# Kernel optimization log

Measured on AMD Instinct MI355X. Metric: run time of the kernel, lower is better.

## Reference

```python
import jax, jax.numpy as jnp
import numpy as np

N, E, D_IN, H, L, C = 50000, 800000, 500, 256, 4, 7
ALPHA, GAMMA, EPS = 0.5, 0.5, 0.1  # self-loop weight, parallel-edge weight, FAConv eps
LN_EPS = 1e-5


def setup_inputs() -> dict:
    key = jax.random.key(0)
    ks = jax.random.split(key, 8)
    x = jax.random.normal(ks[0], (N, D_IN), jnp.float32)
    src = jax.random.randint(ks[1], (E,), 0, N, jnp.int32)
    dst = jax.random.randint(ks[2], (E,), 0, N, jnp.int32)
    dst = jnp.where(dst == src, (dst + 1) % N, dst)  # ensure no self-loops (remove_self_loops is then a no-op)
    edge_index = jnp.stack([src, dst])
    s_in = 1.0 / np.sqrt(D_IN)
    s_h = 1.0 / np.sqrt(H)
    W_init = jax.random.uniform(ks[3], (H, D_IN), jnp.float32, -s_in, s_in)
    b_init = jnp.zeros((H,), jnp.float32)
    att_l = jax.random.uniform(ks[4], (L, H), jnp.float32, -s_h, s_h)
    att_r = jax.random.uniform(ks[5], (L, H), jnp.float32, -s_h, s_h)
    ln_g = jnp.ones((L, H), jnp.float32)
    ln_b = jnp.zeros((L, H), jnp.float32)
    W_last = jax.random.uniform(ks[6], (C, H), jnp.float32, -s_h, s_h)
    b_last = jnp.zeros((C,), jnp.float32)
    return dict(x=x, edge_index=edge_index, W_init=W_init, b_init=b_init,
                att_l=att_l, att_r=att_r, ln_g=ln_g, ln_b=ln_b,
                W_last=W_last, b_last=b_last)


def _layernorm(x, g, b):
    mu = jnp.mean(x, axis=-1, keepdims=True)
    var = jnp.var(x, axis=-1, keepdims=True)
    return (x - mu) * jax.lax.rsqrt(var + LN_EPS) * g + b


def reference(x, edge_index, W_init, b_init, att_l, att_r, ln_g, ln_b, W_last, b_last):
    num_nodes = x.shape[0]
    num_edges = edge_index.shape[1]
    x = x @ W_init.T + b_init  # [N, H]
    x0 = x
    # add self-loops after parallel edges
    loop = jnp.arange(num_nodes, dtype=edge_index.dtype)
    src = jnp.concatenate([edge_index[0], loop])
    dst = jnp.concatenate([edge_index[1], loop])
    ew = jnp.concatenate([jnp.full((num_edges,), GAMMA, x.dtype),
                          jnp.full((num_nodes,), ALPHA, x.dtype)])
    for i in range(L):
        # FAConv: alpha_e = tanh(att_l.x_src + att_r.x_dst); msg = x_src * alpha_e * ew
        al = x @ att_l[i]  # [N]
        ar = x @ att_r[i]  # [N]
        a_e = jnp.tanh(al[src] + ar[dst]) * ew  # [E+N]
        msg = x[src] * a_e[:, None]            # [E+N, H]
        agg = jax.ops.segment_sum(msg, dst, num_segments=num_nodes)
        x = agg + EPS * x0
        if i != L - 1:
            x = _layernorm(jax.nn.relu(x), ln_g[i], ln_b[i])
            # F.dropout with p=0.0 is identity
    emb = x @ W_last.T + b_last  # [N, C]
    return emb, jax.nn.log_softmax(emb, axis=1)
```

## Files before the change

kernel.cpp:

```cpp
#include <hip/hip_runtime.h>
#include <hip/hip_fp16.h>

#define N_NODES 50000
#define N_EDGES 800000
#define D_IN_K  500
#define K_PAD   512
#define H_DIM   256
#define N_CLS   7
#define ALPHA_W 0.5f
#define GAMMA_W 0.5f
#define EPS_W   0.1f
#define LN_EPS_W 1e-5f

#define SCAN_B 256
#define SCAN_NB ((N_NODES + SCAN_B - 1) / SCAN_B)

typedef unsigned short u16;
typedef unsigned int   u32;
typedef _Float16 f16;
typedef __attribute__((ext_vector_type(8))) _Float16 f16x8;
typedef __attribute__((ext_vector_type(4))) float    f32x4;
typedef __attribute__((ext_vector_type(8))) unsigned short u16x8;

__device__ __forceinline__ float h2f(u16 v) {
    __half h;
    *reinterpret_cast<u16*>(&h) = v;
    return __half2float(h);
}
__device__ __forceinline__ u16 f2h(float f) {
    __half h = __float2half_rn(f);
    return *reinterpret_cast<u16*>(&h);
}
__device__ __forceinline__ int clampN(int v) {
    return (v < 0) ? 0 : ((v >= N_NODES) ? N_NODES - 1 : v);
}

__device__ __forceinline__ void fma_mix_row(float* acc, u16x8 v, float c) {
    uint4 p = *reinterpret_cast<const uint4*>(&v);
    asm("v_fma_mix_f32 %0, %1, %2, %0 op_sel:[0,0,0] op_sel_hi:[1,0,0]" : "+v"(acc[0]) : "v"(p.x), "v"(c));
    asm("v_fma_mix_f32 %0, %1, %2, %0 op_sel:[1,0,0] op_sel_hi:[1,0,0]" : "+v"(acc[1]) : "v"(p.x), "v"(c));
    asm("v_fma_mix_f32 %0, %1, %2, %0 op_sel:[0,0,0] op_sel_hi:[1,0,0]" : "+v"(acc[2]) : "v"(p.y), "v"(c));
    asm("v_fma_mix_f32 %0, %1, %2, %0 op_sel:[1,0,0] op_sel_hi:[1,0,0]" : "+v"(acc[3]) : "v"(p.y), "v"(c));
    asm("v_fma_mix_f32 %0, %1, %2, %0 op_sel:[0,0,0] op_sel_hi:[1,0,0]" : "+v"(acc[4]) : "v"(p.z), "v"(c));
    asm("v_fma_mix_f32 %0, %1, %2, %0 op_sel:[1,0,0] op_sel_hi:[1,0,0]" : "+v"(acc[5]) : "v"(p.z), "v"(c));
    asm("v_fma_mix_f32 %0, %1, %2, %0 op_sel:[0,0,0] op_sel_hi:[1,0,0]" : "+v"(acc[6]) : "v"(p.w), "v"(c));
    asm("v_fma_mix_f32 %0, %1, %2, %0 op_sel:[1,0,0] op_sel_hi:[1,0,0]" : "+v"(acc[7]) : "v"(p.w), "v"(c));
}

__global__ __launch_bounds__(256) void sentinel_kernel(float* out, int n) {
    int i = blockIdx.x * blockDim.x + threadIdx.x;
    if (i < n) out[i] = 2.0f;
}

__global__ __launch_bounds__(256) void zero_kernel(int* p, int n) {
    int i = blockIdx.x * blockDim.x + threadIdx.x;
    if (i < n) p[i] = 0;
}

__global__ __launch_bounds__(256) void hist_kernel(const int* __restrict__ dst, int* __restrict__ deg, int e) {
    int i = blockIdx.x * blockDim.x + threadIdx.x;
    if (i < e) atomicAdd(&deg[clampN(dst[i])], 1);
}

__global__ __launch_bounds__(SCAN_B) void scan_a(const int* __restrict__ deg, int* __restrict__ row_ptr,
                                                 int* __restrict__ bsum) {
    __shared__ int sdata[SCAN_B];
    int t = threadIdx.x;
    int i = blockIdx.x * SCAN_B + t;
    int v = (i < N_NODES) ? deg[i] : 0;
    sdata[t] = v;
    __syncthreads();
#pragma unroll
    for (int off = 1; off < SCAN_B; off <<= 1) {
        int a = (t >= off) ? sdata[t - off] : 0;
        __syncthreads();
        sdata[t] += a;
        __syncthreads();
    }
    if (i < N_NODES) row_ptr[i] = sdata[t] - v;
    if (t == SCAN_B - 1) bsum[blockIdx.x] = sdata[t];
}

__global__ __launch_bounds__(SCAN_B) void scan_b(int* __restrict__ bsum, int* __restrict__ boff,
                                                 int* __restrict__ row_ptr) {
    __shared__ int sdata[SCAN_B];
    int t = threadIdx.x;
    int v = (t < SCAN_NB) ? bsum[t] : 0;
    sdata[t] = v;
    __syncthreads();
#pragma unroll
    for (int off = 1; off < SCAN_B; off <<= 1) {
        int a = (t >= off) ? sdata[t - off] : 0;
        __syncthreads();
        sdata[t] += a;
        __syncthreads();
    }
    if (t < SCAN_NB) boff[t] = sdata[t] - v;
    if (t == SCAN_B - 1) row_ptr[N_NODES] = sdata[t];
}

__global__ __launch_bounds__(SCAN_B) void scan_c(int* __restrict__ row_ptr, const int* __restrict__ boff) {
    int i = blockIdx.x * SCAN_B + threadIdx.x;
    if (i < N_NODES) row_ptr[i] += boff[blockIdx.x];
}

__global__ __launch_bounds__(256) void scatter_kernel(const int* __restrict__ src, const int* __restrict__ dst,
                                                      const int* __restrict__ row_ptr, int* __restrict__ deg,
                                                      int* __restrict__ srcS, int e) {
    int i = blockIdx.x * blockDim.x + threadIdx.x;
    if (i < e) {
        int d = clampN(dst[i]);
        int old = atomicSub(&deg[d], 1);
        int pos = row_ptr[d] + old - 1;
        if (pos >= 0 && pos < e) srcS[pos] = clampN(src[i]);
    }
}

__global__ __launch_bounds__(256) void convert_w(const float* __restrict__ W, f16* __restrict__ W16) {
    int i = blockIdx.x * 256 + threadIdx.x;
    int n = i >> 9, k = i & (K_PAD - 1);
    W16[i] = (k < D_IN_K) ? (f16)W[n * D_IN_K + k] : (f16)0.f;
}

#define GW_STRIDE 520
#define GA_BUF    (16 * GW_STRIDE)

__device__ __forceinline__ f16x8 stage_load(const float* __restrict__ X, int tile, int r, int sc) {
    const float* p = X + (long)(tile * 16 + r) * D_IN_K + sc;
    f16x8 v;
    if (sc + 8 <= D_IN_K) {
        float4 lo = *(const float4*)(p);
        float4 hi = *(const float4*)(p + 4);
        v[0] = (f16)lo.x; v[1] = (f16)lo.y; v[2] = (f16)lo.z; v[3] = (f16)lo.w;
        v[4] = (f16)hi.x; v[5] = (f16)hi.y; v[6] = (f16)hi.z; v[7] = (f16)hi.w;
    } else {
#pragma unroll
        for (int t = 0; t < 8; t++)
            v[t] = (sc + t < D_IN_K) ? (f16)p[t] : (f16)0.f;
    }
    return v;
}

__global__ __launch_bounds__(1024) void mfma_gemm5(const float* __restrict__ X,
                                                   const f16* __restrict__ W16,
                                                   const float* __restrict__ bias,
                                                   u16* __restrict__ out) {
    __shared__ __align__(16) f16 alds[2 * GA_BUF];

    int tid  = threadIdx.x;
    int w    = tid >> 6;
    int lane = tid & 63;
    int m    = lane & 15;
    int quad = lane >> 4;
    int h    = w * 16 + m;

    f16x8 bfrag[16];
    {
        const f16* wb = W16 + (long)h * K_PAD + quad * 8;
#pragma unroll
        for (int kc = 0; kc < 16; kc++)
            bfrag[kc] = *(const f16x8*)(wb + kc * 32);
    }
    float bv = bias[h];

    int sr = w;
    int sc = lane * 8;

    int nt = N_NODES / 16;
    int t  = blockIdx.x;
    int buf = 0;

    if (t < nt) {
        f16x8 sv = stage_load(X, t, sr, sc);
        *(f16x8*)&alds[sr * GW_STRIDE + sc] = sv;
    }
    __syncthreads();

    while (t < nt) {
        int tn = t + (int)gridDim.x;
        bool hn = (tn < nt);
        f16x8 nsv;
        if (hn) nsv = stage_load(X, tn, sr, sc);

        f32x4 acc = (f32x4){0.f, 0.f, 0.f, 0.f};
        const f16* ab = &alds[buf * GA_BUF + m * GW_STRIDE + quad * 8];
#pragma unroll
        for (int kc = 0; kc < 16; kc++) {
            f16x8 a = *(const f16x8*)(ab + kc * 32);
            acc = __builtin_amdgcn_mfma_f32_16x16x32_f16(a, bfrag[kc], acc, 0, 0, 0);
        }

        long nb = (long)t * 16 + quad * 4;
#pragma unroll
        for (int r = 0; r < 4; r++)
            out[(nb + r) * H_DIM + h] = f2h(acc[r] + bv);

        if (hn) *(f16x8*)&alds[(buf ^ 1) * GA_BUF + sr * GW_STRIDE + sc] = nsv;
        __syncthreads();
        buf ^= 1;
        t = tn;
    }
}

__global__ __launch_bounds__(256) void alar_kernel(const u16* __restrict__ x,
                                                   const float* __restrict__ attl,
                                                   const float* __restrict__ attr,
                                                   float* __restrict__ al, float* __restrict__ ar, int n) {
    int w = (blockIdx.x * blockDim.x + threadIdx.x) >> 6;
    int lane = threadIdx.x & 63;
    if (w >= n) return;
    int col = lane * 4;
    ushort4 xv = *(const ushort4*)(x + (long)w * H_DIM + col);
    float4 lv = *(const float4*)(attl + col);
    float4 rv = *(const float4*)(attr + col);
    float x0 = h2f(xv.x), x1 = h2f(xv.y), x2 = h2f(xv.z), x3 = h2f(xv.w);
    float pl = x0 * lv.x + x1 * lv.y + x2 * lv.z + x3 * lv.w;
    float pr = x0 * rv.x + x1 * rv.y + x2 * rv.z + x3 * rv.w;
#pragma unroll
    for (int off = 32; off >= 1; off >>= 1) {
        pl += __shfl_xor(pl, off);
        pr += __shfl_xor(pr, off);
    }
    if (lane == 0) { al[w] = pl; ar[w] = pr; }
}

__global__ __launch_bounds__(256) void layer_kernel5(const u16* __restrict__ xin,
                                                     const u16* __restrict__ x0,
                                                     const float* __restrict__ alIn,
                                                     float* __restrict__ alOut,
                                                     float* __restrict__ ar,
                                                     const int* __restrict__ row_ptr,
                                                     const int* __restrict__ srcS,
                                                     const float* __restrict__ g,
                                                     const float* __restrict__ b,
                                                     const float* __restrict__ attlN,
                                                     const float* __restrict__ attrN,
                                                     u16* __restrict__ xout,
                                                     const float* __restrict__ Wl,
                                                     const float* __restrict__ bl,
                                                     float* __restrict__ outF,
                                                     int n, int mode) {
    int pair = (blockIdx.x * 256 + threadIdx.x) >> 6;
    int lane = threadIdx.x & 63;
    int half = lane >> 5;
    int sub  = lane & 31;
    int w = pair * 2 + half;
    if (w >= n) w = n - 1;
    int col = sub * 8;

    float arn = ar[w];
    float aself = ALPHA_W * tanhf(alIn[w] + arn);

    float acc[8];
    {
        u16x8 xs  = *(const u16x8*)(xin + (long)w * H_DIM + col);
        u16x8 x0v = *(const u16x8*)(x0  + (long)w * H_DIM + col);
#pragma unroll
        for (int k = 0; k < 8; k++) acc[k] = aself * h2f(xs[k]) + EPS_W * h2f(x0v[k]);
    }

    int e0 = row_ptr[w], e1 = row_ptr[w + 1];
    int d  = e1 - e0;
    int dmax = max(d, __shfl(d, lane ^ 32));

    for (int cb = 0; cb < dmax; cb += 32) {
        int cnt  = d - cb;
        int cmax = dmax - cb; if (cmax > 32) cmax = 32;
        int s = 0; float a = 0.f;
        if (sub < cnt) {
            s = clampN(srcS[e0 + cb + sub]);
            a = GAMMA_W * tanhf(alIn[s] + arn);
        }
        int hb = half << 5;
        for (int j = 0; j < cmax; j += 4) {
            int   s0 = __shfl(s, hb + j),     s1 = __shfl(s, hb + j + 1);
            int   s2 = __shfl(s, hb + j + 2), s3 = __shfl(s, hb + j + 3);
            float c0 = __shfl(a, hb + j),     c1 = __shfl(a, hb + j + 1);
            float c2 = __shfl(a, hb + j + 2), c3 = __shfl(a, hb + j + 3);
            u16x8 v0 = *(const u16x8*)(xin + (long)s0 * H_DIM + col);
            u16x8 v1 = *(const u16x8*)(xin + (long)s1 * H_DIM + col);
            u16x8 v2 = *(const u16x8*)(xin + (long)s2 * H_DIM + col);
            u16x8 v3 = *(const u16x8*)(xin + (long)s3 * H_DIM + col);
            fma_mix_row(acc, v0, c0);
            fma_mix_row(acc, v1, c1);
            fma_mix_row(acc, v2, c2);
            fma_mix_row(acc, v3, c3);
        }
    }

    if (mode == 0) {
        float v[8];
        float sum = 0.f, sq = 0.f;
#pragma unroll
        for (int k = 0; k < 8; k++) {
            v[k] = fmaxf(acc[k], 0.f);
            sum += v[k];
            sq  += v[k] * v[k];
        }
#pragma unroll
        for (int off = 16; off >= 1; off >>= 1) {
            sum += __shfl_xor(sum, off);
            sq  += __shfl_xor(sq, off);
        }
        float mu = sum * (1.f / 256.f);
        float var = fmaxf(sq * (1.f / 256.f) - mu * mu, 0.f);
        float rstd = rsqrtf(var + LN_EPS_W);
        float4 ga = *(const float4*)(g + col);
        float4 gb = *(const float4*)(g + col + 4);
        float4 ba = *(const float4*)(b + col);
        float4 bb = *(const float4*)(b + col + 4);
        float gg[8]  = {ga.x, ga.y, ga.z, ga.w, gb.x, gb.y, gb.z, gb.w};
        float bbv[8] = {ba.x, ba.y, ba.z, ba.w, bb.x, bb.y, bb.z, bb.w};
        float4 la = *(const float4*)(attlN + col);
        float4 lb = *(const float4*)(attlN + col + 4);
        float4 ra = *(const float4*)(attrN + col);
        float4 rb = *(const float4*)(attrN + col + 4);
        float ll[8] = {la.x, la.y, la.z, la.w, lb.x, lb.y, lb.z, lb.w};
        float rr[8] = {ra.x, ra.y, ra.z, ra.w, rb.x, rb.y, rb.z, rb.w};
        float pl = 0.f, pr = 0.f;
        u16x8 o;
#pragma unroll
        for (int k = 0; k < 8; k++) {
            float val = (v[k] - mu) * rstd * gg[k] + bbv[k];
            o[k] = f2h(val);
            pl += val * ll[k];
            pr += val * rr[k];
        }
#pragma unroll
        for (int off = 16; off >= 1; off >>= 1) {
            pl += __shfl_xor(pl, off);
            pr += __shfl_xor(pr, off);
        }
        if (sub == 0) { alOut[w] = pl; ar[w] = pr; }
        *(u16x8*)(xout + (long)w * H_DIM + col) = o;
    } else {
        float p[N_CLS];
#pragma unroll
        for (int c = 0; c < N_CLS; c++) {
            const float* wr = Wl + c * H_DIM + col;
            float4 wa = *(const float4*)(wr);
            float4 wb = *(const float4*)(wr + 4);
            p[c] = acc[0] * wa.x + acc[1] * wa.y + acc[2] * wa.z + acc[3] * wa.w
                 + acc[4] * wb.x + acc[5] * wb.y + acc[6] * wb.z + acc[7] * wb.w;
        }
#pragma unroll
        for (int off = 16; off >= 1; off >>= 1) {
#pragma unroll
            for (int c = 0; c < N_CLS; c++) p[c] += __shfl_xor(p[c], off);
        }
        if (sub == 0) {
            float e[N_CLS];
            float m = -1e30f;
#pragma unroll
            for (int c = 0; c < N_CLS; c++) {
                e[c] = p[c] + bl[c];
                m = fmaxf(m, e[c]);
            }
            float sx = 0.f;
#pragma unroll
            for (int c = 0; c < N_CLS; c++) sx += expf(e[c] - m);
            float lse = logf(sx);
#pragma unroll
            for (int c = 0; c < N_CLS; c++) {
                outF[(long)w * N_CLS + c] = e[c];
                outF[(long)N_NODES * N_CLS + (long)w * N_CLS + c] = e[c] - m - lse;
            }
        }
    }
}

extern "C" void kernel_launch(void* const* d_in, const int* in_sizes, int n_in,
                              void* d_out, int out_size, void* d_ws, size_t ws_size,
                              hipStream_t stream) {
    const float* x_in   = (const float*)d_in[0];
    const int*   ei     = (const int*)d_in[1];
    const float* W_init = (const float*)d_in[2];
    const float* b_init = (const float*)d_in[3];
    const float* att_l  = (const float*)d_in[4];
    const float* att_r  = (const float*)d_in[5];
    const float* ln_g   = (const float*)d_in[6];
    const float* ln_b   = (const float*)d_in[7];
    const float* W_last = (const float*)d_in[8];
    const float* b_last = (const float*)d_in[9];
    float* out = (float*)d_out;

    const size_t OFF_X0  = 0;
    const size_t OFF_XA  = 25600000;
    const size_t OFF_XB  = 51200000;
    const size_t OFF_AL  = 76800000;
    const size_t OFF_AR  = 77000000;
    const size_t OFF_DEG = 77200000;
    const size_t OFF_RP  = 77400000;
    const size_t OFF_SRC = 77600064;
    const size_t OFF_BS  = 80800064;
    const size_t OFF_BO  = 80801088;
    const size_t WS_NEED = 80802112;

    if (ws_size < WS_NEED) {
        sentinel_kernel<<<(out_size + 255) / 256, 256, 0, stream>>>(out, out_size);
        return;
    }

    char* ws = (char*)d_ws;
    u16* x0  = (u16*)(ws + OFF_X0);
    u16* xA  = (u16*)(ws + OFF_XA);
    u16* xB  = (u16*)(ws + OFF_XB);
    f16* W16 = (f16*)(ws + OFF_AL);
    float* al  = (float*)(ws + OFF_AL);
    float* ar  = (float*)(ws + OFF_AR);
    float* al2 = (float*)(ws + OFF_DEG);
    int* deg     = (int*)(ws + OFF_DEG);
    int* row_ptr = (int*)(ws + OFF_RP);
    int* srcS    = (int*)(ws + OFF_SRC);
    int* bsum    = (int*)(ws + OFF_BS);
    int* boff    = (int*)(ws + OFF_BO);

    const int* e_src = ei;
    const int* e_dst = ei + N_EDGES;

    int zb = (N_NODES + 255) / 256;
    zero_kernel<<<zb, 256, 0, stream>>>(deg, N_NODES);
    int eb = (N_EDGES + 255) / 256;
    hist_kernel<<<eb, 256, 0, stream>>>(e_dst, deg, N_EDGES);
    scan_a<<<SCAN_NB, SCAN_B, 0, stream>>>(deg, row_ptr, bsum);
    scan_b<<<1, SCAN_B, 0, stream>>>(bsum, boff, row_ptr);
    scan_c<<<SCAN_NB, SCAN_B, 0, stream>>>(row_ptr, boff);
    scatter_kernel<<<eb, 256, 0, stream>>>(e_src, e_dst, row_ptr, deg, srcS, N_EDGES);

    convert_w<<<(H_DIM * K_PAD) / 256, 256, 0, stream>>>(W_init, W16);
    mfma_gemm5<<<256, 1024, 0, stream>>>(x_in, W16, b_init, x0);

    int nb = (N_NODES * 64 + 255) / 256;
    alar_kernel<<<nb, 256, 0, stream>>>(x0, att_l, att_r, al, ar, N_NODES);

    int lb = (N_NODES + 7) / 8;
    const u16* bufs_in[4]   = {x0, xA, xB, xA};
    u16* bufs_out[4]        = {xA, xB, xA, xB};
    const float* al_in[4]   = {al, al2, al, al2};
    float* al_out[4]        = {al2, al, al2, al};
    for (int i = 0; i < 4; i++) {
        int nxt = (i < 3) ? (i + 1) : i;
        layer_kernel5<<<lb, 256, 0, stream>>>(bufs_in[i], x0, al_in[i], al_out[i], ar,
                                              row_ptr, srcS,
                                              ln_g + i * H_DIM, ln_b + i * H_DIM,
                                              att_l + nxt * H_DIM, att_r + nxt * H_DIM,
                                              bufs_out[i], W_last, b_last, out,
                                              N_NODES, (i < 3) ? 0 : 1);
    }
}
```

Baseline: 522.8 us.

## Fuse three-kernel scan into one block; triple-buffer GEMM input staging

The three-pass prefix scan over node degrees is replaced by one 1024-thread block. Each thread serially scans a chunk of about 49 entries, which removes two kernel launches. The input GEMM now prefetches raw fp32 rows two tiles ahead into registers, using a three-slot LDS ring with a single barrier per iteration, to hide global load latency behind MFMA work. The risks are a serial single-block scan with uncoalesced strided reads, plus extra register and LDS pressure in the GEMM.

```diff
diff --git a/kernel.cpp b/kernel.cpp
--- a/kernel.cpp
+++ b/kernel.cpp
@@ -12,9 +12,6 @@
 #define EPS_W   0.1f
 #define LN_EPS_W 1e-5f
 
-#define SCAN_B 256
-#define SCAN_NB ((N_NODES + SCAN_B - 1) / SCAN_B)
-
 typedef unsigned short u16;
 typedef unsigned int   u32;
 typedef _Float16 f16;
@@ -62,46 +59,30 @@
     if (i < e) atomicAdd(&deg[clampN(dst[i])], 1);
 }
 
-__global__ __launch_bounds__(SCAN_B) void scan_a(const int* __restrict__ deg, int* __restrict__ row_ptr,
-                                                 int* __restrict__ bsum) {
-    __shared__ int sdata[SCAN_B];
+__global__ __launch_bounds__(1024) void scan_fused(const int* __restrict__ deg, int* __restrict__ row_ptr) {
+    __shared__ int sdata[1024];
     int t = threadIdx.x;
-    int i = blockIdx.x * SCAN_B + t;
-    int v = (i < N_NODES) ? deg[i] : 0;
-    sdata[t] = v;
+    const int CH = (N_NODES + 1023) / 1024;
+    int beg = t * CH;
+    int end = beg + CH; if (end > N_NODES) end = N_NODES;
+    int s = 0;
+    for (int j = beg; j < end; j++) s += deg[j];
+    sdata[t] = s;
     __syncthreads();
 #pragma unroll
-    for (int off = 1; off < SCAN_B; off <<= 1) {
+    for (int off = 1; off < 1024; off <<= 1) {
         int a = (t >= off) ? sdata[t - off] : 0;
         __syncthreads();
         sdata[t] += a;
         __syncthreads();
     }
-    if (i < N_NODES) row_ptr[i] = sdata[t] - v;
-    if (t == SCAN_B - 1) bsum[blockIdx.x] = sdata[t];
-}
-
-__global__ __launch_bounds__(SCAN_B) void scan_b(int* __restrict__ bsum, int* __restrict__ boff,
-                                                 int* __restrict__ row_ptr) {
-    __shared__ int sdata[SCAN_B];
-    int t = threadIdx.x;
-    int v = (t < SCAN_NB) ? bsum[t] : 0;
-    sdata[t] = v;
-    __syncthreads();
-#pragma unroll
-    for (int off = 1; off < SCAN_B; off <<= 1) {
-        int a = (t >= off) ? sdata[t - off] : 0;
-        __syncthreads();
-        sdata[t] += a;
-        __syncthreads();
-    }
-    if (t < SCAN_NB) boff[t] = sdata[t] - v;
-    if (t == SCAN_B - 1) row_ptr[N_NODES] = sdata[t];
-}
-
-__global__ __launch_bounds__(SCAN_B) void scan_c(int* __restrict__ row_ptr, const int* __restrict__ boff) {
-    int i = blockIdx.x * SCAN_B + threadIdx.x;
-    if (i < N_NODES) row_ptr[i] += boff[blockIdx.x];
+    int run = sdata[t] - s;
+    for (int j = beg; j < end; j++) {
+        int d = deg[j];
+        row_ptr[j] = run;
+        run += d;
+    }
+    if (t == 1023) row_ptr[N_NODES] = sdata[1023];
 }
 
 __global__ __launch_bounds__(256) void scatter_kernel(const int* __restrict__ src, const int* __restrict__ dst,
@@ -125,27 +106,32 @@
 #define GW_STRIDE 520
 #define GA_BUF    (16 * GW_STRIDE)
 
-__device__ __forceinline__ f16x8 stage_load(const float* __restrict__ X, int tile, int r, int sc) {
+__device__ __forceinline__ void raw_load(const float* __restrict__ X, int tile, int r, int sc,
+                                         float4& lo, float4& hi) {
     const float* p = X + (long)(tile * 16 + r) * D_IN_K + sc;
+    if (sc + 8 <= D_IN_K) {
+        lo = *(const float4*)(p);
+        hi = *(const float4*)(p + 4);
+    } else if (sc < D_IN_K) {
+        lo = *(const float4*)(p);
+        hi = make_float4(0.f, 0.f, 0.f, 0.f);
+    } else {
+        lo = make_float4(0.f, 0.f, 0.f, 0.f);
+        hi = make_float4(0.f, 0.f, 0.f, 0.f);
+    }
+}
+__device__ __forceinline__ f16x8 cvt8(float4 lo, float4 hi) {
     f16x8 v;
-    if (sc + 8 <= D_IN_K) {
-        float4 lo = *(const float4*)(p);
-        float4 hi = *(const float4*)(p + 4);
-        v[0] = (f16)lo.x; v[1] = (f16)lo.y; v[2] = (f16)lo.z; v[3] = (f16)lo.w;
-        v[4] = (f16)hi.x; v[5] = (f16)hi.y; v[6] = (f16)hi.z; v[7] = (f16)hi.w;
-    } else {
-#pragma unroll
-        for (int t = 0; t < 8; t++)
-            v[t] = (sc + t < D_IN_K) ? (f16)p[t] : (f16)0.f;
-    }
+    v[0] = (f16)lo.x; v[1] = (f16)lo.y; v[2] = (f16)lo.z; v[3] = (f16)lo.w;
+    v[4] = (f16)hi.x; v[5] = (f16)hi.y; v[6] = (f16)hi.z; v[7] = (f16)hi.w;
     return v;
 }
 
-__global__ __launch_bounds__(1024) void mfma_gemm5(const float* __restrict__ X,
+__global__ __launch_bounds__(1024) void mfma_gemm6(const float* __restrict__ X,
                                                    const f16* __restrict__ W16,
                                                    const float* __restrict__ bias,
                                                    u16* __restrict__ out) {
-    __shared__ __align__(16) f16 alds[2 * GA_BUF];
+    __shared__ __align__(16) f16 alds[3 * GA_BUF];
 
     int tid  = threadIdx.x;
     int w    = tid >> 6;
@@ -166,21 +152,26 @@
     int sr = w;
     int sc = lane * 8;
 
-    int nt = N_NODES / 16;
-    int t  = blockIdx.x;
-    int buf = 0;
-
-    if (t < nt) {
-        f16x8 sv = stage_load(X, t, sr, sc);
-        *(f16x8*)&alds[sr * GW_STRIDE + sc] = sv;
-    }
-    __syncthreads();
-
+    const int nt = N_NODES / 16;
+    const int G  = (int)gridDim.x;
+    int t = blockIdx.x;
+
+    {
+        float4 lo, hi;
+        raw_load(X, t, sr, sc, lo, hi);
+        *(f16x8*)&alds[sr * GW_STRIDE + sc] = cvt8(lo, hi);
+    }
+    float4 lo1, hi1;
+    bool h1 = (t + G < nt);
+    if (h1) raw_load(X, t + G, sr, sc, lo1, hi1);
+
+    int buf = 0, nbuf = 1;
     while (t < nt) {
-        int tn = t + (int)gridDim.x;
-        bool hn = (tn < nt);
-        f16x8 nsv;
-        if (hn) nsv = stage_load(X, tn, sr, sc);
+        bool h2 = (t + 2 * G < nt);
+        float4 lo2, hi2;
+        if (h2) raw_load(X, t + 2 * G, sr, sc, lo2, hi2);
+        if (h1) *(f16x8*)&alds[nbuf * GA_BUF + sr * GW_STRIDE + sc] = cvt8(lo1, hi1);
+        __syncthreads();
 
         f32x4 acc = (f32x4){0.f, 0.f, 0.f, 0.f};
         const f16* ab = &alds[buf * GA_BUF + m * GW_STRIDE + quad * 8];
@@ -189,16 +180,14 @@
             f16x8 a = *(const f16x8*)(ab + kc * 32);
             acc = __builtin_amdgcn_mfma_f32_16x16x32_f16(a, bfrag[kc], acc, 0, 0, 0);
         }
-
         long nb = (long)t * 16 + quad * 4;
 #pragma unroll
         for (int r = 0; r < 4; r++)
             out[(nb + r) * H_DIM + h] = f2h(acc[r] + bv);
 
-        if (hn) *(f16x8*)&alds[(buf ^ 1) * GA_BUF + sr * GW_STRIDE + sc] = nsv;
-        __syncthreads();
-        buf ^= 1;
-        t = tn;
+        lo1 = lo2; hi1 = hi2; h1 = h2;
+        t += G;
+        buf = nbuf; nbuf = (nbuf + 1) % 3;
     }
 }
 
@@ -412,8 +401,6 @@
     int* deg     = (int*)(ws + OFF_DEG);
     int* row_ptr = (int*)(ws + OFF_RP);
     int* srcS    = (int*)(ws + OFF_SRC);
-    int* bsum    = (int*)(ws + OFF_BS);
-    int* boff    = (int*)(ws + OFF_BO);
 
     const int* e_src = ei;
     const int* e_dst = ei + N_EDGES;
@@ -422,13 +409,11 @@
     zero_kernel<<<zb, 256, 0, stream>>>(deg, N_NODES);
     int eb = (N_EDGES + 255) / 256;
     hist_kernel<<<eb, 256, 0, stream>>>(e_dst, deg, N_EDGES);
-    scan_a<<<SCAN_NB, SCAN_B, 0, stream>>>(deg, row_ptr, bsum);
-    scan_b<<<1, SCAN_B, 0, stream>>>(bsum, boff, row_ptr);
-    scan_c<<<SCAN_NB, SCAN_B, 0, stream>>>(row_ptr, boff);
+    scan_fused<<<1, 1024, 0, stream>>>(deg, row_ptr);
     scatter_kernel<<<eb, 256, 0, stream>>>(e_src, e_dst, row_ptr, deg, srcS, N_EDGES);
 
     convert_w<<<(H_DIM * K_PAD) / 256, 256, 0, stream>>>(W_init, W16);
-    mfma_gemm5<<<256, 1024, 0, stream>>>(x_in, W16, b_init, x0);
+    mfma_gemm6<<<256, 1024, 0, stream>>>(x_in, W16, b_init, x0);
 
     int nb = (N_NODES * 64 + 255) / 256;
     alar_kernel<<<nb, 256, 0, stream>>>(x0, att_l, att_r, al, ar, N_NODES);
```

Measured after the change: 587.9 us. 12.5% more time.
